# Optimization experiments

Hardware: AMD Instinct MI355X
Metric: run time of the kernel (lower is better)

The kernel has to match this reference:

```python
import jax, jax.numpy as jnp
import numpy as np

N, E, ND, ED, H, L = 50000, 800000, 64, 32, 128, 4
MIN = 2 * H + H + 1  # message MLP input dim = 385
EPS = 1e-5


def _layernorm(x, w, b):
    mu = x.mean(-1, keepdims=True)
    var = ((x - mu) ** 2).mean(-1, keepdims=True)
    return (x - mu) / jnp.sqrt(var + EPS) * w + b


def setup_inputs() -> dict:
    key = jax.random.key(0)
    ks = jax.random.split(key, 40)

    def w(k, shape):
        return jax.random.normal(k, shape, jnp.float32) / np.sqrt(shape[-2]).astype(np.float32)

    inp = {
        "node_features": jax.random.normal(ks[0], (N, ND), jnp.float32),
        "edge_features": jax.random.normal(ks[1], (E, ED), jnp.float32),
        "congestion": jax.random.uniform(ks[2], (N,), jnp.float32),
        "edge_index": jax.random.randint(ks[3], (2, E), 0, N),
        "unrouted_mask": jax.random.randint(ks[4], (N,), 0, 2).astype(jnp.bool_),
        "enc_node_w": w(ks[5], (ND, H)), "enc_node_b": jnp.zeros(H),
        "enc_edge_w": w(ks[6], (ED, H)), "enc_edge_b": jnp.zeros(H),
        "msg_w1": w(ks[7], (L, MIN, H)), "msg_b1": jnp.zeros((L, H)),
        "msg_w2": w(ks[8], (L, H, H)), "msg_b2": jnp.zeros((L, H)),
        "upd_w1": w(ks[9], (L, 2 * H, H)), "upd_b1": jnp.zeros((L, H)),
        "upd_w2": w(ks[10], (L, H, H)), "upd_b2": jnp.zeros((L, H)),
        "ln_w": jnp.ones((L, H)), "ln_b": jnp.zeros((L, H)),
        "unr_w1": w(ks[11], (1, H)), "unr_b1": jnp.zeros(H),
        "unr_w2": w(ks[12], (H, H)), "unr_b2": jnp.zeros(H),
        "ro_w1": w(ks[13], (2 * H, H)), "ro_b1": jnp.zeros(H),
        "ro_w2": w(ks[14], (H, H // 2)), "ro_b2": jnp.zeros(H // 2),
        "ro_w3": w(ks[15], (H // 2, 1)), "ro_b3": jnp.zeros(1),
    }
    return inp


def reference(node_features, edge_features, congestion, edge_index, unrouted_mask,
              enc_node_w, enc_node_b, enc_edge_w, enc_edge_b,
              msg_w1, msg_b1, msg_w2, msg_b2,
              upd_w1, upd_b1, upd_w2, upd_b2,
              ln_w, ln_b,
              unr_w1, unr_b1, unr_w2, unr_b2,
              ro_w1, ro_b1, ro_w2, ro_b2, ro_w3, ro_b3):
    n = node_features.shape[0]
    src, dst = edge_index[0], edge_index[1]

    x = node_features @ enc_node_w + enc_node_b            # [N, H]
    ea = edge_features @ enc_edge_w + enc_edge_b           # [E, H]
    cong_src = congestion[src][:, None]                    # [E, 1]

    for l in range(msg_w1.shape[0]):
        # message: gather src/dst features, concat with edge attr + congestion
        m_in = jnp.concatenate([x[src], x[dst], ea, cong_src], axis=-1)  # [E, 385]
        m = jax.nn.relu(m_in @ msg_w1[l] + msg_b1[l]) @ msg_w2[l] + msg_b2[l]  # [E, H]
        agg = jax.ops.segment_sum(m, dst, num_segments=n)  # scatter_add over dst
        u_in = jnp.concatenate([x, agg], axis=-1)          # [N, 2H]
        x_new = jax.nn.relu(u_in @ upd_w1[l] + upd_b1[l]) @ upd_w2[l] + upd_b2[l]
        x = _layernorm(x + x_new, ln_w[l], ln_b[l])        # dropout = identity (eval)

    graph_embed = x.mean(axis=0, keepdims=True)            # [1, H] (batch=None branch)
    unrouted_frac = unrouted_mask.astype(jnp.float32).mean()[None, None]  # [1, 1]
    unr = jax.nn.relu(unrouted_frac @ unr_w1 + unr_b1) @ unr_w2 + unr_b2  # [1, H]
    combined = jnp.concatenate([graph_embed, unr], axis=-1)  # [1, 2H]
    h = jax.nn.relu(combined @ ro_w1 + ro_b1)
    h = jax.nn.relu(h @ ro_w2 + ro_b2)
    out = jax.nn.sigmoid(h @ ro_w3 + ro_b3)                # [1, 1]
    return out.squeeze(-1)                                 # [1]
```

## Files before the change

kernel.cpp:

```cpp
#include <hip/hip_runtime.h>
#include <hip/hip_fp16.h>
#include <math.h>

#define NN 50000
#define EE 800000

typedef _Float16 half8 __attribute__((ext_vector_type(8)));
typedef __fp16 fp16x2 __attribute__((ext_vector_type(2)));
typedef float floatx4 __attribute__((ext_vector_type(4)));

__global__ void fold_kernel(const float* __restrict__ ew, const float* __restrict__ eb,
                            const float* __restrict__ w1, const float* __restrict__ b1,
                            float* __restrict__ Wc, float* __restrict__ b1f) {
  int l = blockIdx.y, c = blockIdx.x, j = threadIdx.x;
  __shared__ float row[128];
  const float* w1l = w1 + (size_t)l * 385 * 128;
  if (c < 32) {
    row[j] = ew[c * 128 + j];
    __syncthreads();
    float acc = 0.f;
    for (int k = 0; k < 128; k++) acc += row[k] * w1l[(256 + k) * 128 + j];
    Wc[((size_t)l * 32 + c) * 128 + j] = acc;
  } else {
    row[j] = eb[j];
    __syncthreads();
    float acc = b1[l * 128 + j];
    for (int k = 0; k < 128; k++) acc += row[k] * w1l[(256 + k) * 128 + j];
    b1f[l * 128 + j] = acc;
  }
}

__global__ void prep_w(const float* __restrict__ src, _Float16* __restrict__ dst,
                       int K, int perm) {
  int l = blockIdx.y;
  int lane = threadIdx.x;
  int kc = blockIdx.x >> 3, nt = blockIdx.x & 7;
  int n = nt * 16 + (lane & 15);
  int k0 = kc * 32 + (lane >> 4) * 8;
  const float* s = src + (size_t)l * K * 128;
  _Float16 out[8];
  for (int j = 0; j < 8; j++) {
    int k = k0 + j;
    int ks = perm ? ((k & 7) * 16 + (k >> 3)) : k;
    out[j] = (_Float16)s[(size_t)ks * 128 + n];
  }
  _Float16* d = dst + (((size_t)l * gridDim.x + blockIdx.x) * 64 + lane) * 8;
  *(half8*)d = *(half8*)out;
}

__global__ void prep_cong(const float* __restrict__ mw1, _Float16* __restrict__ w1cp) {
  int l = blockIdx.x, p = threadIdx.x;
  int col = (p & 7) * 16 + (p >> 3);
  w1cp[l * 128 + p] = (_Float16)mw1[((size_t)l * 385 + 384) * 128 + col];
}

__global__ void hist_kernel(const int* __restrict__ dstv, int* __restrict__ counts) {
  int e = blockIdx.x * 256 + threadIdx.x;
  if (e < EE) atomicAdd(&counts[dstv[e]], 1);
}

__global__ void scan1_kernel(const int* __restrict__ counts, int* __restrict__ offs,
                             int* __restrict__ bsum) {
  __shared__ int ws[16];
  int t = threadIdx.x, lane = t & 63, w = t >> 6;
  int i = blockIdx.x * 1024 + t;
  int v = (i < NN) ? counts[i] : 0;
  int s = v;
  for (int off = 1; off < 64; off <<= 1) {
    int u = __shfl_up(s, off);
    if (lane >= off) s += u;
  }
  if (lane == 63) ws[w] = s;
  __syncthreads();
  if (w == 0) {
    int u = (lane < 16) ? ws[lane] : 0;
    for (int off = 1; off < 16; off <<= 1) {
      int x = __shfl_up(u, off);
      if (lane >= off && lane < 16) u += x;
    }
    if (lane < 16) ws[lane] = u;
  }
  __syncthreads();
  int wbase = (w > 0) ? ws[w - 1] : 0;
  if (i < NN) offs[i] = wbase + s - v;
  if (t == 0) bsum[blockIdx.x] = ws[15];
}

__global__ void scan2_kernel(int* __restrict__ bsum) {
  int t = threadIdx.x;
  int v = (t < 49) ? bsum[t] : 0;
  int s = v;
  for (int off = 1; off < 64; off <<= 1) {
    int u = __shfl_up(s, off);
    if (t >= off) s += u;
  }
  if (t < 49) bsum[t] = s - v;
}

__global__ void slot1_kernel(const int* __restrict__ dstv, const int* __restrict__ offs,
                             const int* __restrict__ bsum, int* __restrict__ cursor,
                             int* __restrict__ einv) {
  int e = blockIdx.x * 256 + threadIdx.x;
  if (e >= EE) return;
  int d = dstv[e];
  int p = offs[d] + bsum[d >> 10] + atomicAdd(&cursor[d], 1);
  einv[p] = e;
}

__global__ void slot2_kernel(const int* __restrict__ einv, const int* __restrict__ srcv,
                             const int* __restrict__ dstv, const float* __restrict__ ef,
                             int2* __restrict__ meta, _Float16* __restrict__ efh) {
  int p = blockIdx.x * 256 + threadIdx.x;
  if (p >= EE) return;
  int e = einv[p];
  int2 m;
  m.x = srcv[e];
  m.y = dstv[e];
  meta[p] = m;
  const float* sp = ef + (size_t)e * 32;
  _Float16* dp = efh + (size_t)p * 32;
  for (int i = 0; i < 4; i++) {
    float4 f = *(const float4*)(sp + i * 8);
    float4 g = *(const float4*)(sp + i * 8 + 4);
    half8 v;
    v[0] = (_Float16)f.x; v[1] = (_Float16)f.y; v[2] = (_Float16)f.z; v[3] = (_Float16)f.w;
    v[4] = (_Float16)g.x; v[5] = (_Float16)g.y; v[6] = (_Float16)g.z; v[7] = (_Float16)g.w;
    *(half8*)(dp + i * 8) = v;
  }
}

__global__ void enc_mfma(const float* __restrict__ nf, const _Float16* __restrict__ Wenc,
                         const float* __restrict__ bn, _Float16* __restrict__ xh,
                         const _Float16* __restrict__ WSa, const _Float16* __restrict__ WSb,
                         const float* __restrict__ b1f,
                         _Float16* __restrict__ Sh, _Float16* __restrict__ Dh,
                         _Float16* __restrict__ aggz) {
  __shared__ __align__(16) _Float16 hs[4][16][136];
  int t = threadIdx.x, wave = t >> 6, lane = t & 63;
  int quad = lane >> 4, l15 = lane & 15;
  long nb0 = (long)blockIdx.x * 64 + wave * 16;
  long rn = nb0 + l15;
  if (rn >= NN) rn = NN - 1;

  {
    long zn = (long)blockIdx.x * 64 + (t >> 2);
    if (zn < NN) {
      float4* p = (float4*)(aggz + (long)blockIdx.x * 64 * 128 + t * 32);
      float4 z = {};
      p[0] = z; p[1] = z; p[2] = z; p[3] = z;
    }
  }

  floatx4 acc[8] = {};
  for (int kc = 0; kc < 2; kc++) {
    const float* p = nf + rn * 64 + kc * 32 + quad * 8;
    float4 f0 = *(const float4*)p;
    float4 f1 = *(const float4*)(p + 4);
    half8 a;
    a[0] = (_Float16)f0.x; a[1] = (_Float16)f0.y;
    a[2] = (_Float16)f0.z; a[3] = (_Float16)f0.w;
    a[4] = (_Float16)f1.x; a[5] = (_Float16)f1.y;
    a[6] = (_Float16)f1.z; a[7] = (_Float16)f1.w;
    const _Float16* bp = Wenc + (size_t)(kc * 8) * 512 + lane * 8;
    for (int nt = 0; nt < 8; nt++) {
      half8 b = *(const half8*)(bp + nt * 512);
      acc[nt] = __builtin_amdgcn_mfma_f32_16x16x32_f16(a, b, acc[nt], 0, 0, 0);
    }
  }
  float bv[8];
  for (int nt = 0; nt < 8; nt++) bv[nt] = bn[nt * 16 + l15];
  for (int reg = 0; reg < 4; reg++) {
    long n = nb0 + quad * 4 + reg;
    bool ok = n < NN;
    for (int nt = 0; nt < 8; nt++) {
      _Float16 v = (_Float16)(acc[nt][reg] + bv[nt]);
      if (ok) xh[n * 128 + nt * 16 + l15] = v;
      hs[wave][quad * 4 + reg][nt * 16 + l15] = v;
    }
  }

  {
    floatx4 as_[8] = {}, ad[8] = {};
#pragma unroll
    for (int kc = 0; kc < 4; kc++) {
      half8 a = *(const half8*)&hs[wave][l15][kc * 32 + quad * 8];
      const _Float16* bpa = WSa + (size_t)(kc * 8) * 512 + lane * 8;
      const _Float16* bpb = WSb + (size_t)(kc * 8) * 512 + lane * 8;
#pragma unroll
      for (int nt = 0; nt < 8; nt++) {
        half8 ba = *(const half8*)(bpa + nt * 512);
        half8 bbq = *(const half8*)(bpb + nt * 512);
        as_[nt] = __builtin_amdgcn_mfma_f32_16x16x32_f16(a, ba, as_[nt], 0, 0, 0);
        ad[nt] = __builtin_amdgcn_mfma_f32_16x16x32_f16(a, bbq, ad[nt], 0, 0, 0);
      }
    }
    float bfv[8];
    for (int nt = 0; nt < 8; nt++) bfv[nt] = b1f[nt * 16 + l15];
    for (int reg = 0; reg < 4; reg++) {
      long n = nb0 + quad * 4 + reg;
      if (n < NN) {
        half8 hsv, hdv;
        for (int nt = 0; nt < 8; nt++) {
          hsv[nt] = (_Float16)as_[nt][reg];
          hdv[nt] = (_Float16)(ad[nt][reg] + bfv[nt]);
        }
        *(half8*)(Sh + n * 128 + l15 * 8) = hsv;
        *(half8*)(Dh + n * 128 + l15 * 8) = hdv;
      }
    }
  }
}

__global__ __launch_bounds__(256, 3) void msg_kernel(
    const _Float16* __restrict__ Sh, const _Float16* __restrict__ Dh,
    const _Float16* __restrict__ efh, const int2* __restrict__ meta,
    const float* __restrict__ cong,
    const _Float16* __restrict__ Wcp, const _Float16* __restrict__ Wp2,
    const _Float16* __restrict__ w1cp, const float* __restrict__ b2,
    __half* __restrict__ agg) {
  __shared__ __align__(16) _Float16 As[128][136];
  __shared__ int s_src[128], s_dst[128];
  __shared__ float s_cg[128];
  int t = threadIdx.x, wave = t >> 6, lane = t & 63;
  int quad = lane >> 4, l15 = lane & 15;
  long eb0 = (long)blockIdx.x * 128;
  int web = wave * 32;

  if (t < 128) {
    int2 m = meta[eb0 + t];
    s_src[t] = m.x;
    s_dst[t] = m.y;
    s_cg[t] = cong[m.x];
  }
  half8 wcl = *(const half8*)(w1cp + l15 * 8);
  half8 av0 = *(const half8*)(efh + (size_t)(eb0 + web + l15) * 32 + quad * 8);
  half8 av1 = *(const half8*)(efh + (size_t)(eb0 + web + 16 + l15) * 32 + quad * 8);
  __syncthreads();

  half8 sv[8], dv[8];
#pragma unroll
  for (int mtl = 0; mtl < 2; mtl++)
#pragma unroll
    for (int reg = 0; reg < 4; reg++) {
      int r = web + mtl * 16 + quad * 4 + reg;
      sv[mtl * 4 + reg] = *(const half8*)(Sh + (size_t)s_src[r] * 128 + l15 * 8);
      dv[mtl * 4 + reg] = *(const half8*)(Dh + (size_t)s_dst[r] * 128 + l15 * 8);
    }

#pragma unroll
  for (int mtl = 0; mtl < 2; mtl++) {
    half8 a = mtl ? av1 : av0;
    floatx4 e[8] = {};
#pragma unroll
    for (int nt = 0; nt < 8; nt++) {
      half8 b = *(const half8*)(Wcp + (size_t)nt * 512 + lane * 8);
      e[nt] = __builtin_amdgcn_mfma_f32_16x16x32_f16(a, b, e[nt], 0, 0, 0);
    }
#pragma unroll
    for (int reg = 0; reg < 4; reg++) {
      int r = web + mtl * 16 + quad * 4 + reg;
      _Float16 cgh = (_Float16)s_cg[r];
      half8 v = sv[mtl * 4 + reg] + dv[mtl * 4 + reg];
      half8 e8;
#pragma unroll
      for (int i = 0; i < 4; i++) {
        fp16x2 p = __builtin_amdgcn_cvt_pkrtz(e[2 * i][reg], e[2 * i + 1][reg]);
        e8[2 * i] = (_Float16)p[0];
        e8[2 * i + 1] = (_Float16)p[1];
      }
      v += e8;
      v += wcl * cgh;
#pragma unroll
      for (int i = 0; i < 8; i++) v[i] = v[i] > (_Float16)0 ? v[i] : (_Float16)0;
      *(half8*)&As[r][l15 * 8] = v;
    }
  }
  __syncthreads();

  int nb = wave * 2;
  floatx4 acc2[8][2] = {};
  __builtin_amdgcn_s_setprio(1);
#pragma unroll
  for (int kc = 0; kc < 4; kc++) {
    const _Float16* bp = Wp2 + ((size_t)(kc * 8 + nb)) * 512 + lane * 8;
    half8 b0 = *(const half8*)bp;
    half8 b1v = *(const half8*)(bp + 512);
#pragma unroll
    for (int mt = 0; mt < 8; mt++) {
      half8 a = *(const half8*)&As[mt * 16 + l15][kc * 32 + quad * 8];
      acc2[mt][0] = __builtin_amdgcn_mfma_f32_16x16x32_f16(a, b0, acc2[mt][0], 0, 0, 0);
      acc2[mt][1] = __builtin_amdgcn_mfma_f32_16x16x32_f16(a, b1v, acc2[mt][1], 0, 0, 0);
    }
  }
  __builtin_amdgcn_s_setprio(0);
  __syncthreads();

  {
    float c0 = b2[nb * 16 + l15], c1 = b2[(nb + 1) * 16 + l15];
#pragma unroll
    for (int mt = 0; mt < 8; mt++)
#pragma unroll
      for (int reg = 0; reg < 4; reg++) {
        int row = mt * 16 + quad * 4 + reg;
        As[row][nb * 16 + l15] = (_Float16)(acc2[mt][0][reg] + c0);
        As[row][(nb + 1) * 16 + l15] = (_Float16)(acc2[mt][1][reg] + c1);
      }
  }
  __syncthreads();

  {
    int cp = t & 63;
    int q8 = t >> 6;
    int r0 = q8 * 32;
    __half2 vals[32];
#pragma unroll
    for (int i = 0; i < 32; i++) vals[i] = *(__half2*)&As[r0 + i][cp * 2];
    int cur = s_dst[r0];
    __half2 acc = __float2half2_rn(0.f);
    for (int i = 0; i < 32; i++) {
      int d = s_dst[r0 + i];
      if (d != cur) {
        unsafeAtomicAdd((__half2*)(agg + (long)cur * 128 + cp * 2), acc);
        acc = __float2half2_rn(0.f);
        cur = d;
      }
      acc = __hadd2(acc, vals[i]);
    }
    unsafeAtomicAdd((__half2*)(agg + (long)cur * 128 + cp * 2), acc);
  }
}

__global__ __launch_bounds__(256, 3) void upd_kernel(
    _Float16* __restrict__ xh, _Float16* __restrict__ agg,
    const _Float16* __restrict__ Wp1, const _Float16* __restrict__ Wp2,
    const float* __restrict__ b1, const float* __restrict__ b2,
    const float* __restrict__ g, const float* __restrict__ bb,
    const _Float16* __restrict__ WSa, const _Float16* __restrict__ WSb,
    const float* __restrict__ b1f,
    _Float16* __restrict__ Sh, _Float16* __restrict__ Dh) {
  __shared__ __align__(16) _Float16 hs[4][16][136];
  int t = threadIdx.x, wave = t >> 6, lane = t & 63;
  int quad = lane >> 4, l15 = lane & 15;
  long nb0 = (long)blockIdx.x * 64 + wave * 16;

  floatx4 acc[8] = {};
  {
    long n = nb0 + l15;
    long rn = n < NN ? n : NN - 1;
    for (int kc = 0; kc < 8; kc++) {
      half8 a;
      if (kc < 4) {
        a = *(const half8*)(xh + rn * 128 + kc * 32 + quad * 8);
      } else {
        a = *(const half8*)(agg + rn * 128 + (kc - 4) * 32 + quad * 8);
      }
      const _Float16* bp = Wp1 + (size_t)(kc * 8) * 512 + lane * 8;
      for (int nt = 0; nt < 8; nt++) {
        half8 b = *(const half8*)(bp + nt * 512);
        acc[nt] = __builtin_amdgcn_mfma_f32_16x16x32_f16(a, b, acc[nt], 0, 0, 0);
      }
    }
  }

  float bbv[8];
  for (int nt = 0; nt < 8; nt++) bbv[nt] = b1[nt * 16 + l15];
  for (int reg = 0; reg < 4; reg++) {
    half8 hv;
    for (int nt = 0; nt < 8; nt++)
      hv[nt] = (_Float16)fmaxf(acc[nt][reg] + bbv[nt], 0.f);
    *(half8*)&hs[wave][quad * 4 + reg][l15 * 8] = hv;
  }
  __syncthreads();

  floatx4 acc2[8] = {};
  for (int kc = 0; kc < 4; kc++) {
    half8 a = *(const half8*)&hs[wave][l15][kc * 32 + quad * 8];
    const _Float16* bp = Wp2 + (size_t)(kc * 8) * 512 + lane * 8;
    for (int nt = 0; nt < 8; nt++) {
      half8 b = *(const half8*)(bp + nt * 512);
      acc2[nt] = __builtin_amdgcn_mfma_f32_16x16x32_f16(a, b, acc2[nt], 0, 0, 0);
    }
  }

  float b2v[8], gv[8], bv[8];
  for (int nt = 0; nt < 8; nt++) {
    int col = nt * 16 + l15;
    b2v[nt] = b2[col]; gv[nt] = g[col]; bv[nt] = bb[col];
  }
  bool fuse = (WSa != nullptr);
  for (int reg = 0; reg < 4; reg++) {
    long n = nb0 + quad * 4 + reg;
    bool ok = n < NN;
    long rn = ok ? n : NN - 1;
    float y[8];
    float s = 0.f;
    for (int nt = 0; nt < 8; nt++) {
      y[nt] = (float)xh[rn * 128 + nt * 16 + l15] + acc2[nt][reg] + b2v[nt];
      s += y[nt];
    }
    s += __shfl_xor(s, 1); s += __shfl_xor(s, 2);
    s += __shfl_xor(s, 4); s += __shfl_xor(s, 8);
    float mu = s * (1.f / 128.f);
    float q = 0.f;
    for (int nt = 0; nt < 8; nt++) {
      y[nt] -= mu;
      q += y[nt] * y[nt];
    }
    q += __shfl_xor(q, 1); q += __shfl_xor(q, 2);
    q += __shfl_xor(q, 4); q += __shfl_xor(q, 8);
    float rstd = rsqrtf(q * (1.f / 128.f) + 1e-5f);
    for (int nt = 0; nt < 8; nt++) {
      _Float16 o = (_Float16)(y[nt] * rstd * gv[nt] + bv[nt]);
      if (ok) xh[n * 128 + nt * 16 + l15] = o;
      if (fuse) hs[wave][quad * 4 + reg][nt * 16 + l15] = o;
    }
  }

  if (fuse) {
    floatx4 as_[8] = {}, ad[8] = {};
#pragma unroll
    for (int kc = 0; kc < 4; kc++) {
      half8 a = *(const half8*)&hs[wave][l15][kc * 32 + quad * 8];
      const _Float16* bpa = WSa + (size_t)(kc * 8) * 512 + lane * 8;
      const _Float16* bpb = WSb + (size_t)(kc * 8) * 512 + lane * 8;
#pragma unroll
      for (int nt = 0; nt < 8; nt++) {
        half8 ba = *(const half8*)(bpa + nt * 512);
        half8 bbq = *(const half8*)(bpb + nt * 512);
        as_[nt] = __builtin_amdgcn_mfma_f32_16x16x32_f16(a, ba, as_[nt], 0, 0, 0);
        ad[nt] = __builtin_amdgcn_mfma_f32_16x16x32_f16(a, bbq, ad[nt], 0, 0, 0);
      }
    }
    float bfv[8];
    for (int nt = 0; nt < 8; nt++) bfv[nt] = b1f[nt * 16 + l15];
    for (int reg = 0; reg < 4; reg++) {
      long n = nb0 + quad * 4 + reg;
      if (n < NN) {
        half8 hsv, hdv;
        for (int nt = 0; nt < 8; nt++) {
          hsv[nt] = (_Float16)as_[nt][reg];
          hdv[nt] = (_Float16)(ad[nt][reg] + bfv[nt]);
        }
        *(half8*)(Sh + n * 128 + l15 * 8) = hsv;
        *(half8*)(Dh + n * 128 + l15 * 8) = hdv;
      }
    }

    long zn = (long)blockIdx.x * 64 + (t >> 2);
    if (zn < NN) {
      float4* p = (float4*)(agg + (long)blockIdx.x * 64 * 128 + t * 32);
      float4 z = {};
      p[0] = z; p[1] = z; p[2] = z; p[3] = z;
    }
  }
}

__global__ void reduce_kernel(const _Float16* __restrict__ xh,
                              const int* __restrict__ umask, float* __restrict__ red) {
  int t = threadIdx.x;
  long base = (long)blockIdx.x * 196;
  int j = t & 127, half = t >> 7;
  float acc = 0.f;
  for (int i = 0; i < 98; i++) {
    long n = base + half + 2L * i;
    if (n < NN) acc += (float)xh[n * 128 + j];
  }
  __shared__ float sr[2][128];
  __shared__ float sm[4];
  sr[half][j] = acc;
  float mv = 0.f;
  {
    long n = base + t;
    if (t < 196 && n < NN) mv = (float)umask[n];
  }
  for (int off = 32; off; off >>= 1) mv += __shfl_xor(mv, off);
  if ((t & 63) == 0) sm[t >> 6] = mv;
  __syncthreads();
  if (t < 128) atomicAdd(&red[t], sr[0][t] + sr[1][t]);
  if (t == 0) atomicAdd(&red[128], sm[0] + sm[1] + sm[2] + sm[3]);
}

__global__ void readout_kernel(const float* __restrict__ red,
                               const float* __restrict__ xw1, const float* __restrict__ xb1,
                               const float* __restrict__ xw2, const float* __restrict__ xb2,
                               const float* __restrict__ rw1, const float* __restrict__ rb1,
                               const float* __restrict__ rw2, const float* __restrict__ rb2,
                               const float* __restrict__ rw3, const float* __restrict__ rb3,
                               float* __restrict__ out) {
  __shared__ float sa[128], sb[128], sc[128];
  int j = threadIdx.x;
  const float inv = 1.f / (float)NN;
  float ge = red[j] * inv;
  float uf = red[128] * inv;
  float u1 = fmaxf(uf * xw1[j] + xb1[j], 0.f);
  sa[j] = u1;
  sb[j] = ge;
  __syncthreads();
  float u2 = xb2[j];
  for (int k = 0; k < 128; k++) u2 += sa[k] * xw2[k * 128 + j];
  sc[j] = u2;
  __syncthreads();
  float h1 = rb1[j];
  for (int k = 0; k < 128; k++) h1 += sb[k] * rw1[k * 128 + j];
  for (int k = 0; k < 128; k++) h1 += sc[k] * rw1[(128 + k) * 128 + j];
  h1 = fmaxf(h1, 0.f);
  __syncthreads();
  sa[j] = h1;
  __syncthreads();
  float h2 = 0.f;
  if (j < 64) {
    h2 = rb2[j];
    for (int k = 0; k < 128; k++) h2 += sa[k] * rw2[k * 64 + j];
    h2 = fmaxf(h2, 0.f);
  }
  __syncthreads();
  if (j < 64) sb[j] = h2;
  __syncthreads();
  if (j == 0) {
    float a = rb3[0];
    for (int k = 0; k < 64; k++) a += sb[k] * rw3[k];
    out[0] = 1.f / (1.f + expf(-a));
  }
}

extern "C" void kernel_launch(void* const* d_in, const int* in_sizes, int n_in,
                              void* d_out, int out_size, void* d_ws, size_t ws_size,
                              hipStream_t stream) {
  const float* nf   = (const float*)d_in[0];
  const float* ef   = (const float*)d_in[1];
  const float* cong = (const float*)d_in[2];
  const int*   eidx = (const int*)d_in[3];
  const int*   um   = (const int*)d_in[4];
  const float* enw  = (const float*)d_in[5];
  const float* enb  = (const float*)d_in[6];
  const float* eew  = (const float*)d_in[7];
  const float* eeb  = (const float*)d_in[8];
  const float* mw1  = (const float*)d_in[9];
  const float* mb1  = (const float*)d_in[10];
  const float* mw2  = (const float*)d_in[11];
  const float* mb2  = (const float*)d_in[12];
  const float* uw1  = (const float*)d_in[13];
  const float* ub1  = (const float*)d_in[14];
  const float* uw2  = (const float*)d_in[15];
  const float* ub2  = (const float*)d_in[16];
  const float* lnw  = (const float*)d_in[17];
  const float* lnb  = (const float*)d_in[18];
  const float* xw1  = (const float*)d_in[19];
  const float* xb1  = (const float*)d_in[20];
  const float* xw2  = (const float*)d_in[21];
  const float* xb2  = (const float*)d_in[22];
  const float* rw1  = (const float*)d_in[23];
  const float* rb1  = (const float*)d_in[24];
  const float* rw2  = (const float*)d_in[25];
  const float* rb2  = (const float*)d_in[26];
  const float* rw3  = (const float*)d_in[27];
  const float* rb3  = (const float*)d_in[28];
  float* out = (float*)d_out;

  char* W = (char*)d_ws;
  _Float16* xh    = (_Float16*)(W + 0);
  __half*   agg   = (__half*)(W + 12800000);
  _Float16* efh   = (_Float16*)(W + 25600000);
  _Float16* Sh    = (_Float16*)(W + 76800000);
  _Float16* Dh    = (_Float16*)(W + 89600000);
  int2*     meta  = (int2*)(W + 102400000);
  int*      einv  = (int*)(W + 108800000);
  int*      counts= (int*)(W + 112000000);
  int*      cursor= (int*)(W + 112200000);
  int*      offs  = (int*)(W + 112400000);
  _Float16* WSa   = (_Float16*)(W + 112600000);
  _Float16* WSb   = (_Float16*)(W + 112731072);
  _Float16* Wcp   = (_Float16*)(W + 112862144);
  _Float16* Wm2   = (_Float16*)(W + 112894912);
  _Float16* Wu1   = (_Float16*)(W + 113025984);
  _Float16* Wu2   = (_Float16*)(W + 113288128);
  _Float16* Wen   = (_Float16*)(W + 113419200);
  float*    Wc    = (float*)(W + 113435584);
  float*    b1f   = (float*)(W + 113501120);
  _Float16* w1cp  = (_Float16*)(W + 113503168);
  float*    red   = (float*)(W + 113504192);
  int*      bsum  = (int*)red;

  const int* srcv = eidx;
  const int* dstv = eidx + EE;

  (void)hipMemsetAsync(counts, 0, 400000, stream);
  hist_kernel<<<3125, 256, 0, stream>>>(dstv, counts);
  scan1_kernel<<<49, 1024, 0, stream>>>(counts, offs, bsum);
  scan2_kernel<<<1, 64, 0, stream>>>(bsum);
  slot1_kernel<<<3125, 256, 0, stream>>>(dstv, offs, bsum, cursor, einv);
  slot2_kernel<<<3125, 256, 0, stream>>>(einv, srcv, dstv, ef, meta, efh);

  fold_kernel<<<dim3(33, 4), 128, 0, stream>>>(eew, eeb, mw1, mb1, Wc, b1f);
  prep_w<<<dim3(8, 4), 64, 0, stream>>>(Wc, Wcp, 32, 0);
  prep_w<<<dim3(32, 4), 64, 0, stream>>>(mw1, WSa, 385, 0);
  prep_w<<<dim3(32, 4), 64, 0, stream>>>(mw1 + 128 * 128, WSb, 385, 0);
  prep_w<<<dim3(32, 4), 64, 0, stream>>>(mw2, Wm2, 128, 1);
  prep_w<<<dim3(64, 4), 64, 0, stream>>>(uw1, Wu1, 256, 0);
  prep_w<<<dim3(32, 4), 64, 0, stream>>>(uw2, Wu2, 128, 1);
  prep_w<<<dim3(16, 1), 64, 0, stream>>>(enw, Wen, 64, 0);
  prep_cong<<<4, 128, 0, stream>>>(mw1, w1cp);
  enc_mfma<<<782, 256, 0, stream>>>(nf, Wen, enb, xh, WSa, WSb, b1f, Sh, Dh,
                                    (_Float16*)agg);

  for (int l = 0; l < 4; l++) {
    msg_kernel<<<6250, 256, 0, stream>>>(
        Sh, Dh, efh, meta, cong,
        Wcp + (size_t)l * 8 * 512, Wm2 + (size_t)l * 32 * 512,
        w1cp + l * 128, mb2 + l * 128, agg);
    bool fuse = (l < 3);
    upd_kernel<<<782, 256, 0, stream>>>(
        xh, (_Float16*)agg,
        Wu1 + (size_t)l * 64 * 512, Wu2 + (size_t)l * 32 * 512,
        ub1 + l * 128, ub2 + l * 128, lnw + l * 128, lnb + l * 128,
        fuse ? WSa + (size_t)(l + 1) * 32 * 512 : (const _Float16*)nullptr,
        fuse ? WSb + (size_t)(l + 1) * 32 * 512 : (const _Float16*)nullptr,
        fuse ? b1f + (l + 1) * 128 : (const float*)nullptr,
        Sh, Dh);
  }

  (void)hipMemsetAsync(red, 0, 129 * sizeof(float), stream);
  reduce_kernel<<<256, 256, 0, stream>>>(xh, um, red);
  readout_kernel<<<1, 128, 0, stream>>>(red, xw1, xb1, xw2, xb2,
                                        rw1, rb1, rw2, rb2, rw3, rb3, out);
}
```

Before: 848.0 us.

## Make msg_kernel wave-independent with per-wave LDS tiles and shuffled edge metadata

Each wave now owns 32 edges end to end. Edge metadata is held in registers and broadcast with __shfl instead of being staged in shared memory. The second GEMM computes all 128 output columns for the wave's own 32 rows, so As is split per wave and every __syncthreads barrier is gone. This removes block-level synchronization stalls, at the cost of larger per-wave accumulators (2x8 floatx4) and more B-matrix loads per wave, which raises register pressure.

New measurement: 892.1 us. 5.2% more time.

```diff
diff --git a/kernel.cpp b/kernel.cpp
--- a/kernel.cpp
+++ b/kernel.cpp
@@ -218,33 +218,34 @@
     const _Float16* __restrict__ Wcp, const _Float16* __restrict__ Wp2,
     const _Float16* __restrict__ w1cp, const float* __restrict__ b2,
     __half* __restrict__ agg) {
-  __shared__ __align__(16) _Float16 As[128][136];
-  __shared__ int s_src[128], s_dst[128];
-  __shared__ float s_cg[128];
+  __shared__ __align__(16) _Float16 As[4][32][136];
   int t = threadIdx.x, wave = t >> 6, lane = t & 63;
   int quad = lane >> 4, l15 = lane & 15;
-  long eb0 = (long)blockIdx.x * 128;
-  int web = wave * 32;
-
-  if (t < 128) {
-    int2 m = meta[eb0 + t];
-    s_src[t] = m.x;
-    s_dst[t] = m.y;
-    s_cg[t] = cong[m.x];
-  }
+  long eb0 = (long)blockIdx.x * 128 + wave * 32;
+
+  int msrc = 0, mdst = 0;
+  float mcg = 0.f;
+  if (lane < 32) {
+    int2 m = meta[eb0 + lane];
+    msrc = m.x;
+    mdst = m.y;
+    mcg = cong[m.x];
+  }
+
   half8 wcl = *(const half8*)(w1cp + l15 * 8);
-  half8 av0 = *(const half8*)(efh + (size_t)(eb0 + web + l15) * 32 + quad * 8);
-  half8 av1 = *(const half8*)(efh + (size_t)(eb0 + web + 16 + l15) * 32 + quad * 8);
-  __syncthreads();
+  half8 av0 = *(const half8*)(efh + (size_t)(eb0 + l15) * 32 + quad * 8);
+  half8 av1 = *(const half8*)(efh + (size_t)(eb0 + 16 + l15) * 32 + quad * 8);
 
   half8 sv[8], dv[8];
 #pragma unroll
   for (int mtl = 0; mtl < 2; mtl++)
 #pragma unroll
     for (int reg = 0; reg < 4; reg++) {
-      int r = web + mtl * 16 + quad * 4 + reg;
-      sv[mtl * 4 + reg] = *(const half8*)(Sh + (size_t)s_src[r] * 128 + l15 * 8);
-      dv[mtl * 4 + reg] = *(const half8*)(Dh + (size_t)s_dst[r] * 128 + l15 * 8);
+      int r = mtl * 16 + quad * 4 + reg;
+      int s = __shfl(msrc, r);
+      int d = __shfl(mdst, r);
+      sv[mtl * 4 + reg] = *(const half8*)(Sh + (size_t)s * 128 + l15 * 8);
+      dv[mtl * 4 + reg] = *(const half8*)(Dh + (size_t)d * 128 + l15 * 8);
     }
 
 #pragma unroll
@@ -258,8 +259,8 @@
     }
 #pragma unroll
     for (int reg = 0; reg < 4; reg++) {
-      int r = web + mtl * 16 + quad * 4 + reg;
-      _Float16 cgh = (_Float16)s_cg[r];
+      int r = mtl * 16 + quad * 4 + reg;
+      _Float16 cgh = (_Float16)__shfl(mcg, r);
       half8 v = sv[mtl * 4 + reg] + dv[mtl * 4 + reg];
       half8 e8;
 #pragma unroll
@@ -272,53 +273,50 @@
       v += wcl * cgh;
 #pragma unroll
       for (int i = 0; i < 8; i++) v[i] = v[i] > (_Float16)0 ? v[i] : (_Float16)0;
-      *(half8*)&As[r][l15 * 8] = v;
-    }
-  }
-  __syncthreads();
-
-  int nb = wave * 2;
-  floatx4 acc2[8][2] = {};
+      *(half8*)&As[wave][r][l15 * 8] = v;
+    }
+  }
+
+  floatx4 acc2[2][8] = {};
   __builtin_amdgcn_s_setprio(1);
 #pragma unroll
   for (int kc = 0; kc < 4; kc++) {
-    const _Float16* bp = Wp2 + ((size_t)(kc * 8 + nb)) * 512 + lane * 8;
-    half8 b0 = *(const half8*)bp;
-    half8 b1v = *(const half8*)(bp + 512);
-#pragma unroll
-    for (int mt = 0; mt < 8; mt++) {
-      half8 a = *(const half8*)&As[mt * 16 + l15][kc * 32 + quad * 8];
-      acc2[mt][0] = __builtin_amdgcn_mfma_f32_16x16x32_f16(a, b0, acc2[mt][0], 0, 0, 0);
-      acc2[mt][1] = __builtin_amdgcn_mfma_f32_16x16x32_f16(a, b1v, acc2[mt][1], 0, 0, 0);
+    half8 a0 = *(const half8*)&As[wave][l15][kc * 32 + quad * 8];
+    half8 a1 = *(const half8*)&As[wave][16 + l15][kc * 32 + quad * 8];
+    const _Float16* bp = Wp2 + (size_t)(kc * 8) * 512 + lane * 8;
+#pragma unroll
+    for (int nt = 0; nt < 8; nt++) {
+      half8 b = *(const half8*)(bp + nt * 512);
+      acc2[0][nt] = __builtin_amdgcn_mfma_f32_16x16x32_f16(a0, b, acc2[0][nt], 0, 0, 0);
+      acc2[1][nt] = __builtin_amdgcn_mfma_f32_16x16x32_f16(a1, b, acc2[1][nt], 0, 0, 0);
     }
   }
   __builtin_amdgcn_s_setprio(0);
-  __syncthreads();
 
   {
-    float c0 = b2[nb * 16 + l15], c1 = b2[(nb + 1) * 16 + l15];
-#pragma unroll
-    for (int mt = 0; mt < 8; mt++)
-#pragma unroll
-      for (int reg = 0; reg < 4; reg++) {
-        int row = mt * 16 + quad * 4 + reg;
-        As[row][nb * 16 + l15] = (_Float16)(acc2[mt][0][reg] + c0);
-        As[row][(nb + 1) * 16 + l15] = (_Float16)(acc2[mt][1][reg] + c1);
-      }
-  }
-  __syncthreads();
+    float bv2[8];
+#pragma unroll
+    for (int nt = 0; nt < 8; nt++) bv2[nt] = b2[nt * 16 + l15];
+#pragma unroll
+    for (int mtl = 0; mtl < 2; mtl++)
+#pragma unroll
+      for (int nt = 0; nt < 8; nt++)
+#pragma unroll
+        for (int reg = 0; reg < 4; reg++) {
+          int row = mtl * 16 + quad * 4 + reg;
+          As[wave][row][nt * 16 + l15] = (_Float16)(acc2[mtl][nt][reg] + bv2[nt]);
+        }
+  }
 
   {
-    int cp = t & 63;
-    int q8 = t >> 6;
-    int r0 = q8 * 32;
+    int cp = lane;
     __half2 vals[32];
 #pragma unroll
-    for (int i = 0; i < 32; i++) vals[i] = *(__half2*)&As[r0 + i][cp * 2];
-    int cur = s_dst[r0];
+    for (int i = 0; i < 32; i++) vals[i] = *(__half2*)&As[wave][i][cp * 2];
+    int cur = __shfl(mdst, 0);
     __half2 acc = __float2half2_rn(0.f);
     for (int i = 0; i < 32; i++) {
-      int d = s_dst[r0 + i];
+      int d = __shfl(mdst, i);
       if (d != cur) {
         unsafeAtomicAdd((__half2*)(agg + (long)cur * 128 + cp * 2), acc);
         acc = __float2half2_rn(0.f);
```

## Fuse final reduction into update kernel and halve msg_kernel block size

Applied to the files above, without the earlier changes.

Removes the separate reduce_kernel. The unrouted-mask sum moves into the encoder kernel, and the column sums of the final node features are accumulated inside the last update kernel. Separately, msg_kernel is restructured to use 128-thread blocks covering 64 edges, with each wave computing 4 column tiles over 4 row tiles instead of 2 over 8. This changes occupancy and the register/LDS footprint. Using fp16-rounded outputs for the mean and issuing more atomics per block are the trade-offs.

Result: slower. 886.8 us (+4.6%).

```diff
diff --git a/kernel.cpp b/kernel.cpp
--- a/kernel.cpp
+++ b/kernel.cpp
@@ -134,7 +134,8 @@
                          const _Float16* __restrict__ WSa, const _Float16* __restrict__ WSb,
                          const float* __restrict__ b1f,
                          _Float16* __restrict__ Sh, _Float16* __restrict__ Dh,
-                         _Float16* __restrict__ aggz) {
+                         _Float16* __restrict__ aggz,
+                         const int* __restrict__ um, float* __restrict__ red) {
   __shared__ __align__(16) _Float16 hs[4][16][136];
   int t = threadIdx.x, wave = t >> 6, lane = t & 63;
   int quad = lane >> 4, l15 = lane & 15;
@@ -149,6 +150,13 @@
       float4 z = {};
       p[0] = z; p[1] = z; p[2] = z; p[3] = z;
     }
+  }
+
+  if (t < 64) {
+    long n = (long)blockIdx.x * 64 + t;
+    float mv = (n < NN) ? (float)um[n] : 0.f;
+    for (int off = 32; off; off >>= 1) mv += __shfl_xor(mv, off);
+    if (t == 0) atomicAdd(&red[128], mv);
   }
 
   floatx4 acc[8] = {};
@@ -211,22 +219,22 @@
   }
 }
 
-__global__ __launch_bounds__(256, 3) void msg_kernel(
+__global__ __launch_bounds__(128, 4) void msg_kernel(
     const _Float16* __restrict__ Sh, const _Float16* __restrict__ Dh,
     const _Float16* __restrict__ efh, const int2* __restrict__ meta,
     const float* __restrict__ cong,
     const _Float16* __restrict__ Wcp, const _Float16* __restrict__ Wp2,
     const _Float16* __restrict__ w1cp, const float* __restrict__ b2,
     __half* __restrict__ agg) {
-  __shared__ __align__(16) _Float16 As[128][136];
-  __shared__ int s_src[128], s_dst[128];
-  __shared__ float s_cg[128];
+  __shared__ __align__(16) _Float16 As[64][136];
+  __shared__ int s_src[64], s_dst[64];
+  __shared__ float s_cg[64];
   int t = threadIdx.x, wave = t >> 6, lane = t & 63;
   int quad = lane >> 4, l15 = lane & 15;
-  long eb0 = (long)blockIdx.x * 128;
+  long eb0 = (long)blockIdx.x * 64;
   int web = wave * 32;
 
-  if (t < 128) {
+  if (t < 64) {
     int2 m = meta[eb0 + t];
     s_src[t] = m.x;
     s_dst[t] = m.y;
@@ -277,41 +285,47 @@
   }
   __syncthreads();
 
-  int nb = wave * 2;
-  floatx4 acc2[8][2] = {};
+  int nb = wave * 4;
+  floatx4 acc2[4][4] = {};
   __builtin_amdgcn_s_setprio(1);
 #pragma unroll
   for (int kc = 0; kc < 4; kc++) {
     const _Float16* bp = Wp2 + ((size_t)(kc * 8 + nb)) * 512 + lane * 8;
     half8 b0 = *(const half8*)bp;
     half8 b1v = *(const half8*)(bp + 512);
-#pragma unroll
-    for (int mt = 0; mt < 8; mt++) {
+    half8 b2v = *(const half8*)(bp + 1024);
+    half8 b3v = *(const half8*)(bp + 1536);
+#pragma unroll
+    for (int mt = 0; mt < 4; mt++) {
       half8 a = *(const half8*)&As[mt * 16 + l15][kc * 32 + quad * 8];
       acc2[mt][0] = __builtin_amdgcn_mfma_f32_16x16x32_f16(a, b0, acc2[mt][0], 0, 0, 0);
       acc2[mt][1] = __builtin_amdgcn_mfma_f32_16x16x32_f16(a, b1v, acc2[mt][1], 0, 0, 0);
+      acc2[mt][2] = __builtin_amdgcn_mfma_f32_16x16x32_f16(a, b2v, acc2[mt][2], 0, 0, 0);
+      acc2[mt][3] = __builtin_amdgcn_mfma_f32_16x16x32_f16(a, b3v, acc2[mt][3], 0, 0, 0);
     }
   }
   __builtin_amdgcn_s_setprio(0);
   __syncthreads();
 
   {
-    float c0 = b2[nb * 16 + l15], c1 = b2[(nb + 1) * 16 + l15];
-#pragma unroll
-    for (int mt = 0; mt < 8; mt++)
+    float c[4];
+#pragma unroll
+    for (int ntp = 0; ntp < 4; ntp++) c[ntp] = b2[(nb + ntp) * 16 + l15];
+#pragma unroll
+    for (int mt = 0; mt < 4; mt++)
 #pragma unroll
       for (int reg = 0; reg < 4; reg++) {
         int row = mt * 16 + quad * 4 + reg;
-        As[row][nb * 16 + l15] = (_Float16)(acc2[mt][0][reg] + c0);
-        As[row][(nb + 1) * 16 + l15] = (_Float16)(acc2[mt][1][reg] + c1);
+#pragma unroll
+        for (int ntp = 0; ntp < 4; ntp++)
+          As[row][(nb + ntp) * 16 + l15] = (_Float16)(acc2[mt][ntp][reg] + c[ntp]);
       }
   }
   __syncthreads();
 
   {
-    int cp = t & 63;
-    int q8 = t >> 6;
-    int r0 = q8 * 32;
+    int cp = lane;
+    int r0 = wave * 32;
     __half2 vals[32];
 #pragma unroll
     for (int i = 0; i < 32; i++) vals[i] = *(__half2*)&As[r0 + i][cp * 2];
@@ -337,7 +351,8 @@
     const float* __restrict__ g, const float* __restrict__ bb,
     const _Float16* __restrict__ WSa, const _Float16* __restrict__ WSb,
     const float* __restrict__ b1f,
-    _Float16* __restrict__ Sh, _Float16* __restrict__ Dh) {
+    _Float16* __restrict__ Sh, _Float16* __restrict__ Dh,
+    int do_red, float* __restrict__ red) {
   __shared__ __align__(16) _Float16 hs[4][16][136];
   int t = threadIdx.x, wave = t >> 6, lane = t & 63;
   int quad = lane >> 4, l15 = lane & 15;
@@ -388,6 +403,8 @@
     b2v[nt] = b2[col]; gv[nt] = g[col]; bv[nt] = bb[col];
   }
   bool fuse = (WSa != nullptr);
+  float cs[8];
+  for (int nt = 0; nt < 8; nt++) cs[nt] = 0.f;
   for (int reg = 0; reg < 4; reg++) {
     long n = nb0 + quad * 4 + reg;
     bool ok = n < NN;
@@ -413,6 +430,7 @@
       _Float16 o = (_Float16)(y[nt] * rstd * gv[nt] + bv[nt]);
       if (ok) xh[n * 128 + nt * 16 + l15] = o;
       if (fuse) hs[wave][quad * 4 + reg][nt * 16 + l15] = o;
+      if (do_red) cs[nt] += ok ? (float)o : 0.f;
     }
   }
 
@@ -453,31 +471,20 @@
       p[0] = z; p[1] = z; p[2] = z; p[3] = z;
     }
   }
-}
-
-__global__ void reduce_kernel(const _Float16* __restrict__ xh,
-                              const int* __restrict__ umask, float* __restrict__ red) {
-  int t = threadIdx.x;
-  long base = (long)blockIdx.x * 196;
-  int j = t & 127, half = t >> 7;
-  float acc = 0.f;
-  for (int i = 0; i < 98; i++) {
-    long n = base + half + 2L * i;
-    if (n < NN) acc += (float)xh[n * 128 + j];
-  }
-  __shared__ float sr[2][128];
-  __shared__ float sm[4];
-  sr[half][j] = acc;
-  float mv = 0.f;
-  {
-    long n = base + t;
-    if (t < 196 && n < NN) mv = (float)umask[n];
-  }
-  for (int off = 32; off; off >>= 1) mv += __shfl_xor(mv, off);
-  if ((t & 63) == 0) sm[t >> 6] = mv;
-  __syncthreads();
-  if (t < 128) atomicAdd(&red[t], sr[0][t] + sr[1][t]);
-  if (t == 0) atomicAdd(&red[128], sm[0] + sm[1] + sm[2] + sm[3]);
+
+  if (do_red) {
+    for (int nt = 0; nt < 8; nt++) {
+      cs[nt] += __shfl_xor(cs[nt], 16);
+      cs[nt] += __shfl_xor(cs[nt], 32);
+    }
+    __syncthreads();
+    float* hsF = (float*)hs;
+    if (quad == 0)
+      for (int nt = 0; nt < 8; nt++) hsF[wave * 128 + nt * 16 + l15] = cs[nt];
+    __syncthreads();
+    if (t < 128)
+      atomicAdd(&red[t], hsF[t] + hsF[128 + t] + hsF[256 + t] + hsF[384 + t]);
+  }
 }
 
 __global__ void readout_kernel(const float* __restrict__ red,
@@ -600,11 +607,12 @@
   prep_w<<<dim3(32, 4), 64, 0, stream>>>(uw2, Wu2, 128, 1);
   prep_w<<<dim3(16, 1), 64, 0, stream>>>(enw, Wen, 64, 0);
   prep_cong<<<4, 128, 0, stream>>>(mw1, w1cp);
+  (void)hipMemsetAsync(red, 0, 129 * sizeof(float), stream);
   enc_mfma<<<782, 256, 0, stream>>>(nf, Wen, enb, xh, WSa, WSb, b1f, Sh, Dh,
-                                    (_Float16*)agg);
+                                    (_Float16*)agg, um, red);
 
   for (int l = 0; l < 4; l++) {
-    msg_kernel<<<6250, 256, 0, stream>>>(
+    msg_kernel<<<12500, 128, 0, stream>>>(
         Sh, Dh, efh, meta, cong,
         Wcp + (size_t)l * 8 * 512, Wm2 + (size_t)l * 32 * 512,
         w1cp + l * 128, mb2 + l * 128, agg);
@@ -616,11 +624,9 @@
         fuse ? WSa + (size_t)(l + 1) * 32 * 512 : (const _Float16*)nullptr,
         fuse ? WSb + (size_t)(l + 1) * 32 * 512 : (const _Float16*)nullptr,
         fuse ? b1f + (l + 1) * 128 : (const float*)nullptr,
-        Sh, Dh);
-  }
-
-  (void)hipMemsetAsync(red, 0, 129 * sizeof(float), stream);
-  reduce_kernel<<<256, 256, 0, stream>>>(xh, um, red);
+        Sh, Dh, (l == 3) ? 1 : 0, red);
+  }
+
   readout_kernel<<<1, 128, 0, stream>>>(red, xw1, xb1, xw2, xb2,
                                         rw1, rb1, rw2, rb2, rw3, rb3, out);
 }
```
